# Kernel tuning notes

Hardware: AMD Instinct MI355X
Metric: run time of the kernel (lower is better)

## Reference

```python
import jax, jax.numpy as jnp
import numpy as np

B, S, D, F, E, TOP_K = 4, 2048, 1024, 4096, 8, 2


def setup_inputs() -> dict:
    key = jax.random.key(0)
    ks = jax.random.split(key, 6)
    sd = 1.0 / np.sqrt(D)
    sf = 1.0 / np.sqrt(F)
    return {
        "x": jax.random.normal(ks[0], (B, S, D), dtype=jnp.float32),
        "router_w": jax.random.normal(ks[1], (E, D), dtype=jnp.float32) * sd,
        "router_b": jnp.zeros((E,), dtype=jnp.float32),
        "w1": jax.random.normal(ks[2], (E, F, D), dtype=jnp.float32) * sd,  # Linear(d_model->d_ff) weight [out,in]
        "w2": jax.random.normal(ks[3], (E, D, F), dtype=jnp.float32) * sf,  # Linear(d_ff->d_model)
        "w3": jax.random.normal(ks[4], (E, F, D), dtype=jnp.float32) * sd,
    }


def reference(x, router_w, router_b, w1, w2, w3):
    # Router: softmax over experts, then top-k with renormalized gates.
    logits = jnp.einsum("bsd,ed->bse", x, router_w) + router_b          # [B,S,E]
    probs = jax.nn.softmax(logits, axis=-1)
    topk_p, topk_i = jax.lax.top_k(probs, TOP_K)                         # [B,S,K]
    topk_p = topk_p / jnp.sum(topk_p, axis=-1, keepdims=True)
    # Per-token combine weight for each expert (0 if not selected).
    combine = jnp.sum(jax.nn.one_hot(topk_i, E, dtype=x.dtype) * topk_p[..., None], axis=-2)  # [B,S,E]

    # Note: expert(x*mask)*mask == expert(x)*mask since SwiGLU(0)=0 (no bias).
    out = jnp.zeros_like(x)
    for e in range(E):  # small fixed expert count
        h = jax.nn.silu(jnp.einsum("bsd,fd->bsf", x, w1[e])) * jnp.einsum("bsd,fd->bsf", x, w3[e])
        out = out + combine[..., e:e + 1] * jnp.einsum("bsf,df->bsd", h, w2[e])
    return out
```

## Files before the change

### kernel.cpp

```cpp
#include <hip/hip_runtime.h>
#include <hip/hip_fp16.h>


#define NTOK 8192
#define D_ 1024
#define F_ 4096
#define E_ 8
#define SLOT_CAP 18432

using half8 = __attribute__((ext_vector_type(8))) _Float16;
using half4 = __attribute__((ext_vector_type(4))) _Float16;
using f32x4 = __attribute__((ext_vector_type(4))) float;

__device__ __forceinline__ void gload16(const void* g, void* l) {
  __builtin_amdgcn_global_load_lds((const __attribute__((address_space(1))) void*)g,
                                   (__attribute__((address_space(3))) void*)l, 16, 0, 0);
}

__global__ __launch_bounds__(256) void cvt_kernel(const float* __restrict__ src,
                                                  _Float16* __restrict__ dst, int n4) {
  int i = blockIdx.x * 256 + threadIdx.x;
  int stride = gridDim.x * 256;
  for (; i < n4; i += stride) {
    float4 v = ((const float4*)src)[i];
    half4 h;
    h.x = (_Float16)v.x; h.y = (_Float16)v.y; h.z = (_Float16)v.z; h.w = (_Float16)v.w;
    ((half4*)dst)[i] = h;
  }
}

__global__ __launch_bounds__(256) void cvt_w13_kernel(const float* __restrict__ w1,
                                                      const float* __restrict__ w3,
                                                      _Float16* __restrict__ w13, int n4) {
  int i = blockIdx.x * 256 + threadIdx.x;
  int stride = gridDim.x * 256;
  for (; i < n4; i += stride) {
    int d4 = i & 255;
    int row = i >> 8;
    int e = row >> 12, f = row & 4095;
    size_t vbase = ((size_t)e << 13) | ((size_t)(f >> 4) << 5) | (size_t)(f & 15);
    float4 v1 = ((const float4*)w1)[i];
    float4 v3 = ((const float4*)w3)[i];
    half4 h1, h3;
    h1.x = (_Float16)v1.x; h1.y = (_Float16)v1.y; h1.z = (_Float16)v1.z; h1.w = (_Float16)v1.w;
    h3.x = (_Float16)v3.x; h3.y = (_Float16)v3.y; h3.z = (_Float16)v3.z; h3.w = (_Float16)v3.w;
    ((half4*)w13)[vbase * 256 + d4] = h1;
    ((half4*)w13)[(vbase + 16) * 256 + d4] = h3;
  }
}

__global__ __launch_bounds__(256) void router_kernel(
    const float* __restrict__ x, const float* __restrict__ rw, const float* __restrict__ rbias,
    _Float16* __restrict__ x16, int* __restrict__ tok_e, float* __restrict__ tok_g,
    int* __restrict__ counts) {
  int wv = threadIdx.x >> 6, lane = threadIdx.x & 63;
  int t = blockIdx.x * 4 + wv;
  const float4* xr = (const float4*)(x + (size_t)t * D_);
  float acc[E_];
#pragma unroll
  for (int e = 0; e < E_; ++e) acc[e] = 0.f;
  for (int i = lane; i < D_ / 4; i += 64) {
    float4 xv = xr[i];
    half4 hx;
    hx.x = (_Float16)xv.x; hx.y = (_Float16)xv.y; hx.z = (_Float16)xv.z; hx.w = (_Float16)xv.w;
    ((half4*)(x16 + (size_t)t * D_))[i] = hx;
#pragma unroll
    for (int e = 0; e < E_; ++e) {
      float4 wv4 = ((const float4*)(rw + (size_t)e * D_))[i];
      acc[e] += xv.x * wv4.x + xv.y * wv4.y + xv.z * wv4.z + xv.w * wv4.w;
    }
  }
#pragma unroll
  for (int e = 0; e < E_; ++e) {
#pragma unroll
    for (int off = 32; off > 0; off >>= 1) acc[e] += __shfl_down(acc[e], off);
  }
  if (lane == 0) {
    float p[E_], mx = -1e30f;
#pragma unroll
    for (int e = 0; e < E_; ++e) { p[e] = acc[e] + rbias[e]; mx = fmaxf(mx, p[e]); }
#pragma unroll
    for (int e = 0; e < E_; ++e) p[e] = expf(p[e] - mx);
    int i0 = 0;
#pragma unroll
    for (int e = 1; e < E_; ++e) if (p[e] > p[i0]) i0 = e;
    int i1 = (i0 == 0) ? 1 : 0;
#pragma unroll
    for (int e = 0; e < E_; ++e) if (e != i0 && p[e] > p[i1]) i1 = e;
    float s = p[i0] + p[i1];
    tok_e[t * 2] = i0; tok_e[t * 2 + 1] = i1;
    tok_g[t * 2] = p[i0] / s; tok_g[t * 2 + 1] = p[i1] / s;
    atomicAdd(&counts[i0], 1); atomicAdd(&counts[i1], 1);
  }
}

__global__ void init_kernel(int* slot_token, int* counts, int* cursor) {
  int i = blockIdx.x * 256 + threadIdx.x;
  if (blockIdx.x == 0 && threadIdx.x < E_) { counts[threadIdx.x] = 0; cursor[threadIdx.x] = 0; }
  if (i < SLOT_CAP) slot_token[i] = 0;
}

__global__ void scan_kernel(const int* __restrict__ counts, int* __restrict__ offs) {
  if (threadIdx.x == 0) {
    int o = 0;
    for (int e = 0; e < E_; ++e) { offs[e] = o; o += ((counts[e] + 255) / 256) * 256; }
    offs[E_] = o;
  }
}

__global__ void scatter_kernel(const int* __restrict__ tok_e, const int* __restrict__ offs,
                               int* __restrict__ cursor, int* __restrict__ slot_token,
                               int* __restrict__ slot_of) {
  int i = blockIdx.x * 256 + threadIdx.x;
  if (i >= NTOK * 2) return;
  int e = tok_e[i];
  int pos = offs[e] + atomicAdd(&cursor[e], 1);
  slot_token[pos] = i >> 1;
  slot_of[i] = pos;
}

template <int MODE, int ORD, int KSPLIT, int KD, int NBN, int RPX, int BEROWS>
__global__ __launch_bounds__(512, 2) void moe_gemm_kernel(
    const _Float16* __restrict__ Amat, const _Float16* __restrict__ Bmat,
    const int* __restrict__ slot_token, const int* __restrict__ offs,
    void* __restrict__ outp, void* __restrict__ outp2) {
  constexpr int BM = 256;
  constexpr int MROW = 8;
  constexpr int AH = BM * 32;
  constexpr int BUFH = (BM + 256) * 32;
  constexpr int KL = KD / KSPLIT;
  constexpr int NT = KL / 32;
  __shared__ _Float16 lds[4 * BUFH];

  int id = blockIdx.x;
  int xcd = id & 7, idx = id >> 3;
  int vr, nb;
  if constexpr (ORD == 0) {
    int band = idx / (8 * NBN);
    int i2 = idx - band * (8 * NBN);
    int rib = (RPX - band * 8) < 8 ? (RPX - band * 8) : 8;
    nb = i2 / rib;
    vr = xcd * RPX + band * 8 + (i2 - nb * rib);
  } else {
    nb = idx % NBN;
    vr = xcd * RPX + idx / NBN;
  }
  int rb = vr, ks = 0;
  if constexpr (KSPLIT == 2) { rb = vr >> 1; ks = vr & 1; }
  int row0 = rb * BM;
  if (row0 >= offs[E_]) return;
  int e = 0;
#pragma unroll
  for (int i = 1; i < E_; ++i) if (row0 >= offs[i]) e = i;
  int koff = ks * KL;

  int t = threadIdx.x, l = t & 63, w = t >> 6;
  int wr = w >> 2, wc = w & 3;
  int srow = t >> 2;
  int gsrc8 = ((l & 3) ^ ((l >> 3) & 3)) * 8;

  const _Float16* aP0;
  const _Float16* aP1;
  if constexpr (MODE == 0) {
    int tk0 = slot_token[row0 + srow];
    int tk1 = slot_token[row0 + srow + 128];
    aP0 = Amat + (size_t)tk0 * KD + koff + gsrc8;
    aP1 = Amat + (size_t)tk1 * KD + koff + gsrc8;
  } else {
    aP0 = Amat + (size_t)(row0 + srow) * KD + koff + gsrc8;
    aP1 = Amat + (size_t)(row0 + srow + 128) * KD + koff + gsrc8;
  }
  const _Float16* b0P =
      Bmat + ((size_t)e * BEROWS + (size_t)nb * 256 + srow) * KD + koff + gsrc8;
  const _Float16* b1P = b0P + (size_t)128 * KD;

  int fr = l & 15, kg = l >> 4;
  int swz8 = (kg ^ ((fr >> 1) & 3)) * 8;
  const int rA = (wr * 128 + fr) * 32 + swz8;
  const int rB = AH + (wc * 64 + fr) * 32 + swz8;

  half8 aF[MROW];
  half8 bF[4], bF2[4];
  f32x4 acc[MROW][4];
#pragma unroll
  for (int m = 0; m < MROW; ++m)
#pragma unroll
    for (int n = 0; n < 4; ++n) acc[m][n] = (f32x4){0.f, 0.f, 0.f, 0.f};

#pragma unroll
  for (int tt = 0; tt < 3; ++tt) {
    gload16(aP0 + tt * 32, &lds[tt * BUFH + w * 512]);
    gload16(aP1 + tt * 32, &lds[tt * BUFH + 4096 + w * 512]);
    gload16(b0P + tt * 32, &lds[tt * BUFH + AH + w * 512]);
    gload16(b1P + tt * 32, &lds[tt * BUFH + AH + 4096 + w * 512]);
  }
  asm volatile("s_waitcnt vmcnt(4)" ::: "memory");
  __builtin_amdgcn_s_barrier();
  __builtin_amdgcn_sched_barrier(0);
#pragma unroll
  for (int m = 0; m < MROW; ++m) aF[m] = *(const half8*)&lds[rA + m * 512];
#pragma unroll
  for (int n = 0; n < 4; ++n) bF[n] = *(const half8*)&lds[rB + n * 512];
  __builtin_amdgcn_sched_barrier(0);
  aP0 += 96; aP1 += 96; b0P += 96; b1P += 96;

#define SGB_(m, n) __builtin_amdgcn_sched_group_barrier(m, n, 0)
#define MF4B(mm, BU)                                                                       \
  acc[mm][0] = __builtin_amdgcn_mfma_f32_16x16x32_f16(aF[mm], BU[0], acc[mm][0], 0, 0, 0); \
  acc[mm][1] = __builtin_amdgcn_mfma_f32_16x16x32_f16(aF[mm], BU[1], acc[mm][1], 0, 0, 0); \
  acc[mm][2] = __builtin_amdgcn_mfma_f32_16x16x32_f16(aF[mm], BU[2], acc[mm][2], 0, 0, 0); \
  acc[mm][3] = __builtin_amdgcn_mfma_f32_16x16x32_f16(aF[mm], BU[3], acc[mm][3], 0, 0, 0);

#define GSTEP(U, PRE, WN, BU, BR)                                                 \
  {                                                                               \
    constexpr int bn_ = ((U) + 1) & 3;                                            \
    constexpr int bs_ = ((U) + 3) & 3;                                            \
    __builtin_amdgcn_s_setprio(1);                                                \
    if (PRE) {                                                                    \
      gload16(aP0 + (U) * 32, &lds[bs_ * BUFH + w * 512]);                        \
      gload16(aP1 + (U) * 32, &lds[bs_ * BUFH + 4096 + w * 512]);                 \
      gload16(b0P + (U) * 32, &lds[bs_ * BUFH + AH + w * 512]);                   \
      gload16(b1P + (U) * 32, &lds[bs_ * BUFH + AH + 4096 + w * 512]);            \
    }                                                                             \
    const _Float16* nb_ = &lds[bn_ * BUFH];                                       \
    BR[0] = *(const half8*)(nb_ + rB);                                            \
    BR[1] = *(const half8*)(nb_ + rB + 512);                                      \
    BR[2] = *(const half8*)(nb_ + rB + 1024);                                     \
    BR[3] = *(const half8*)(nb_ + rB + 1536);                                     \
    MF4B(0, BU) aF[0] = *(const half8*)(nb_ + rA);                                \
    MF4B(1, BU) aF[1] = *(const half8*)(nb_ + rA + 512);                          \
    MF4B(2, BU) aF[2] = *(const half8*)(nb_ + rA + 1024);                         \
    MF4B(3, BU) aF[3] = *(const half8*)(nb_ + rA + 1536);                         \
    MF4B(4, BU) aF[4] = *(const half8*)(nb_ + rA + 2048);                         \
    MF4B(5, BU) aF[5] = *(const half8*)(nb_ + rA + 2560);                         \
    MF4B(6, BU) aF[6] = *(const half8*)(nb_ + rA + 3072);                         \
    MF4B(7, BU) aF[7] = *(const half8*)(nb_ + rA + 3584);                         \
    if (PRE) SGB_(0x20, 4);                                                       \
    SGB_(0x100, 4);                                                               \
    SGB_(0x8, 4); SGB_(0x100, 1);                                                 \
    SGB_(0x8, 4); SGB_(0x100, 1);                                                 \
    SGB_(0x8, 4); SGB_(0x100, 1);                                                 \
    SGB_(0x8, 4); SGB_(0x100, 1);                                                 \
    SGB_(0x8, 4); SGB_(0x100, 1);                                                 \
    SGB_(0x8, 4); SGB_(0x100, 1);                                                 \
    SGB_(0x8, 4); SGB_(0x100, 1);                                                 \
    SGB_(0x8, 4); SGB_(0x100, 1);                                                 \
    __builtin_amdgcn_s_setprio(0);                                                \
    if ((WN) >= 0) {                                                              \
      asm volatile("s_waitcnt vmcnt(%0)" ::"i"((WN) >= 0 ? (WN) : 0) : "memory"); \
      __builtin_amdgcn_s_barrier();                                               \
      __builtin_amdgcn_sched_barrier(0);                                          \
    }                                                                             \
  }

  for (int j4 = 0; j4 < NT - 4; j4 += 4) {
    GSTEP(0, true, 4, bF, bF2)
    GSTEP(1, true, 4, bF2, bF)
    GSTEP(2, true, 4, bF, bF2)
    GSTEP(3, true, 4, bF2, bF)
    aP0 += 128; aP1 += 128; b0P += 128; b1P += 128;
  }
  GSTEP(0, true, 4, bF, bF2)
  GSTEP(1, false, 0, bF2, bF)
  GSTEP(2, false, -1, bF, bF2)
  __builtin_amdgcn_s_setprio(1);
  MF4B(0, bF2) MF4B(1, bF2) MF4B(2, bF2) MF4B(3, bF2)
  MF4B(4, bF2) MF4B(5, bF2) MF4B(6, bF2) MF4B(7, bF2)
  __builtin_amdgcn_s_setprio(0);
#undef GSTEP
#undef MF4B
#undef SGB_

  int q4 = kg * 4;
  if constexpr (MODE == 0) {
    _Float16* hb = (_Float16*)outp;
#pragma unroll
    for (int mi = 0; mi < MROW; ++mi) {
      size_t rbase = (size_t)(row0 + wr * 128 + mi * 16 + q4);
#pragma unroll
      for (int p = 0; p < 2; ++p) {
        int fc = nb * 128 + (wc * 2 + p) * 16 + fr;
#pragma unroll
        for (int i = 0; i < 4; ++i) {
          float gv = acc[mi][2 * p][i];
          float hv = gv / (1.f + __expf(-gv)) * acc[mi][2 * p + 1][i];
          hb[(rbase + i) * (size_t)F_ + fc] = (_Float16)hv;
        }
      }
    }
  } else {
    float* yb = (float*)(ks == 0 ? outp : outp2);
#pragma unroll
    for (int mi = 0; mi < MROW; ++mi) {
      size_t rbase = (size_t)(row0 + wr * 128 + mi * 16 + q4);
#pragma unroll
      for (int ni = 0; ni < 4; ++ni) {
        int col = nb * 256 + wc * 64 + ni * 16 + fr;
#pragma unroll
        for (int i = 0; i < 4; ++i)
          yb[(rbase + i) * (size_t)D_ + col] = acc[mi][ni][i];
      }
    }
  }
}

__global__ __launch_bounds__(256) void combine_kernel(
    const float* __restrict__ ya, const float* __restrict__ yb2,
    const int* __restrict__ slot_of, const float* __restrict__ tok_g,
    float* __restrict__ out) {
  int t = blockIdx.x, i = threadIdx.x;
  int s0 = slot_of[t * 2], s1 = slot_of[t * 2 + 1];
  float g0 = tok_g[t * 2], g1 = tok_g[t * 2 + 1];
  float4 a0 = ((const float4*)(ya + (size_t)s0 * D_))[i];
  float4 a1 = ((const float4*)(yb2 + (size_t)s0 * D_))[i];
  float4 b0 = ((const float4*)(ya + (size_t)s1 * D_))[i];
  float4 b1 = ((const float4*)(yb2 + (size_t)s1 * D_))[i];
  float4 r;
  r.x = g0 * (a0.x + a1.x) + g1 * (b0.x + b1.x);
  r.y = g0 * (a0.y + a1.y) + g1 * (b0.y + b1.y);
  r.z = g0 * (a0.z + a1.z) + g1 * (b0.z + b1.z);
  r.w = g0 * (a0.w + a1.w) + g1 * (b0.w + b1.w);
  ((float4*)(out + (size_t)t * D_))[i] = r;
}

extern "C" void kernel_launch(void* const* d_in, const int* in_sizes, int n_in,
                              void* d_out, int out_size, void* d_ws, size_t ws_size,
                              hipStream_t stream) {
  const float* x  = (const float*)d_in[0];
  const float* rw = (const float*)d_in[1];
  const float* rbc = (const float*)d_in[2];
  const float* w1 = (const float*)d_in[3];
  const float* w2 = (const float*)d_in[4];
  const float* w3 = (const float*)d_in[5];
  float* out = (float*)d_out;

  char* ws = (char*)d_ws;
  size_t off = 0;
  auto take = [&](size_t bytes) {
    char* p = ws + off;
    off = (off + bytes + 255) & ~(size_t)255;
    return p;
  };
  _Float16* x16 = (_Float16*)take((size_t)NTOK * D_ * 2);
  _Float16* w13 = (_Float16*)take((size_t)E_ * 2 * F_ * D_ * 2);
  _Float16* w2h = (_Float16*)take((size_t)E_ * D_ * F_ * 2);
  _Float16* hbuf = (_Float16*)take((size_t)SLOT_CAP * F_ * 2);
  float* ybuf = (float*)take((size_t)SLOT_CAP * D_ * 4);
  int* slot_token = (int*)take((size_t)SLOT_CAP * 4);
  int* tok_e = (int*)take((size_t)NTOK * 2 * 4);
  float* tok_g = (float*)take((size_t)NTOK * 2 * 4);
  int* slot_of = (int*)take((size_t)NTOK * 2 * 4);
  int* counts = (int*)take(E_ * 4);
  int* cursor = (int*)take(E_ * 4);
  int* offs = (int*)take((E_ + 1) * 4);
  float* ybuf2 = (float*)w13;

  cvt_w13_kernel<<<4096, 256, 0, stream>>>(w1, w3, w13, E_ * F_ * D_ / 4);
  cvt_kernel<<<4096, 256, 0, stream>>>(w2, w2h, E_ * D_ * F_ / 4);
  init_kernel<<<(SLOT_CAP + 255) / 256, 256, 0, stream>>>(slot_token, counts, cursor);
  router_kernel<<<NTOK / 4, 256, 0, stream>>>(x, rw, rbc, x16, tok_e, tok_g, counts);
  scan_kernel<<<1, 64, 0, stream>>>(counts, offs);
  scatter_kernel<<<(NTOK * 2 + 255) / 256, 256, 0, stream>>>(tok_e, offs, cursor, slot_token, slot_of);
  moe_gemm_kernel<0, 0, 1, 1024, 32, 9, 8192><<<2304, 512, 0, stream>>>(
      x16, w13, slot_token, offs, (void*)hbuf, nullptr);
  moe_gemm_kernel<1, 1, 2, 4096, 4, 18, 1024><<<576, 512, 0, stream>>>(
      hbuf, w2h, slot_token, offs, (void*)ybuf, (void*)ybuf2);
  combine_kernel<<<NTOK, 256, 0, stream>>>(ybuf, ybuf2, slot_of, tok_g, out);
}
```

Baseline: 900.7 us.

## Restructure GEMM main loop into two-phase ping-pong with barriers and reduced fragment registers

Replaces the software-pipelined main loop, which prefetched next-stage A/B fragments interleaved with MFMAs under sched_group_barrier hints, with a two-phase scheme. Each phase loads four A and four B fragments from the current LDS buffer, synchronizes with block barriers and lgkmcnt(0), then issues 16 MFMAs. Global loads are split across the two phases and the vmcnt waits are adjusted to match. This cuts fragment registers (aF 8->4, no double-buffered bF), which may help occupancy, but it adds extra barriers and exposes LDS latency before each MFMA burst.

```diff
diff --git a/kernel.cpp b/kernel.cpp
--- a/kernel.cpp
+++ b/kernel.cpp
@@ -179,8 +179,8 @@
   const int rA = (wr * 128 + fr) * 32 + swz8;
   const int rB = AH + (wc * 64 + fr) * 32 + swz8;
 
-  half8 aF[MROW];
-  half8 bF[4], bF2[4];
+  half8 aF[4];
+  half8 bF[4];
   f32x4 acc[MROW][4];
 #pragma unroll
   for (int m = 0; m < MROW; ++m)
@@ -194,82 +194,79 @@
     gload16(b0P + tt * 32, &lds[tt * BUFH + AH + w * 512]);
     gload16(b1P + tt * 32, &lds[tt * BUFH + AH + 4096 + w * 512]);
   }
-  asm volatile("s_waitcnt vmcnt(4)" ::: "memory");
+  asm volatile("s_waitcnt vmcnt(8)" ::: "memory");
   __builtin_amdgcn_s_barrier();
   __builtin_amdgcn_sched_barrier(0);
-#pragma unroll
-  for (int m = 0; m < MROW; ++m) aF[m] = *(const half8*)&lds[rA + m * 512];
-#pragma unroll
-  for (int n = 0; n < 4; ++n) bF[n] = *(const half8*)&lds[rB + n * 512];
-  __builtin_amdgcn_sched_barrier(0);
   aP0 += 96; aP1 += 96; b0P += 96; b1P += 96;
 
-#define SGB_(m, n) __builtin_amdgcn_sched_group_barrier(m, n, 0)
-#define MF4B(mm, BU)                                                                       \
-  acc[mm][0] = __builtin_amdgcn_mfma_f32_16x16x32_f16(aF[mm], BU[0], acc[mm][0], 0, 0, 0); \
-  acc[mm][1] = __builtin_amdgcn_mfma_f32_16x16x32_f16(aF[mm], BU[1], acc[mm][1], 0, 0, 0); \
-  acc[mm][2] = __builtin_amdgcn_mfma_f32_16x16x32_f16(aF[mm], BU[2], acc[mm][2], 0, 0, 0); \
-  acc[mm][3] = __builtin_amdgcn_mfma_f32_16x16x32_f16(aF[mm], BU[3], acc[mm][3], 0, 0, 0);
-
-#define GSTEP(U, PRE, WN, BU, BR)                                                 \
+#define MF16(BASE)                                                           \
+  _Pragma("unroll") for (int mi = 0; mi < 4; ++mi)                           \
+  _Pragma("unroll") for (int ni = 0; ni < 4; ++ni)                           \
+      acc[(BASE) + mi][ni] = __builtin_amdgcn_mfma_f32_16x16x32_f16(         \
+          aF[mi], bF[ni], acc[(BASE) + mi][ni], 0, 0, 0);
+
+#define STEPP(U, PRE, WN)                                                         \
   {                                                                               \
-    constexpr int bn_ = ((U) + 1) & 3;                                            \
+    constexpr int bi_ = (U) & 3;                                                  \
     constexpr int bs_ = ((U) + 3) & 3;                                            \
-    __builtin_amdgcn_s_setprio(1);                                                \
+    const _Float16* cb_ = &lds[bi_ * BUFH];                                       \
     if (PRE) {                                                                    \
       gload16(aP0 + (U) * 32, &lds[bs_ * BUFH + w * 512]);                        \
       gload16(aP1 + (U) * 32, &lds[bs_ * BUFH + 4096 + w * 512]);                 \
+    }                                                                             \
+    aF[0] = *(const half8*)(cb_ + rA);                                            \
+    aF[1] = *(const half8*)(cb_ + rA + 512);                                      \
+    aF[2] = *(const half8*)(cb_ + rA + 1024);                                     \
+    aF[3] = *(const half8*)(cb_ + rA + 1536);                                     \
+    bF[0] = *(const half8*)(cb_ + rB);                                            \
+    bF[1] = *(const half8*)(cb_ + rB + 512);                                      \
+    bF[2] = *(const half8*)(cb_ + rB + 1024);                                     \
+    bF[3] = *(const half8*)(cb_ + rB + 1536);                                     \
+    __builtin_amdgcn_sched_barrier(0);                                            \
+    __builtin_amdgcn_s_barrier();                                                 \
+    asm volatile("s_waitcnt lgkmcnt(0)" ::: "memory");                            \
+    __builtin_amdgcn_sched_barrier(0);                                            \
+    __builtin_amdgcn_s_setprio(1);                                                \
+    MF16(0)                                                                       \
+    __builtin_amdgcn_s_setprio(0);                                                \
+    __builtin_amdgcn_sched_barrier(0);                                            \
+    __builtin_amdgcn_s_barrier();                                                 \
+    if (PRE) {                                                                    \
       gload16(b0P + (U) * 32, &lds[bs_ * BUFH + AH + w * 512]);                   \
       gload16(b1P + (U) * 32, &lds[bs_ * BUFH + AH + 4096 + w * 512]);            \
     }                                                                             \
-    const _Float16* nb_ = &lds[bn_ * BUFH];                                       \
-    BR[0] = *(const half8*)(nb_ + rB);                                            \
-    BR[1] = *(const half8*)(nb_ + rB + 512);                                      \
-    BR[2] = *(const half8*)(nb_ + rB + 1024);                                     \
-    BR[3] = *(const half8*)(nb_ + rB + 1536);                                     \
-    MF4B(0, BU) aF[0] = *(const half8*)(nb_ + rA);                                \
-    MF4B(1, BU) aF[1] = *(const half8*)(nb_ + rA + 512);                          \
-    MF4B(2, BU) aF[2] = *(const half8*)(nb_ + rA + 1024);                         \
-    MF4B(3, BU) aF[3] = *(const half8*)(nb_ + rA + 1536);                         \
-    MF4B(4, BU) aF[4] = *(const half8*)(nb_ + rA + 2048);                         \
-    MF4B(5, BU) aF[5] = *(const half8*)(nb_ + rA + 2560);                         \
-    MF4B(6, BU) aF[6] = *(const half8*)(nb_ + rA + 3072);                         \
-    MF4B(7, BU) aF[7] = *(const half8*)(nb_ + rA + 3584);                         \
-    if (PRE) SGB_(0x20, 4);                                                       \
-    SGB_(0x100, 4);                                                               \
-    SGB_(0x8, 4); SGB_(0x100, 1);                                                 \
-    SGB_(0x8, 4); SGB_(0x100, 1);                                                 \
-    SGB_(0x8, 4); SGB_(0x100, 1);                                                 \
-    SGB_(0x8, 4); SGB_(0x100, 1);                                                 \
-    SGB_(0x8, 4); SGB_(0x100, 1);                                                 \
-    SGB_(0x8, 4); SGB_(0x100, 1);                                                 \
-    SGB_(0x8, 4); SGB_(0x100, 1);                                                 \
-    SGB_(0x8, 4); SGB_(0x100, 1);                                                 \
+    aF[0] = *(const half8*)(cb_ + rA + 2048);                                     \
+    aF[1] = *(const half8*)(cb_ + rA + 2560);                                     \
+    aF[2] = *(const half8*)(cb_ + rA + 3072);                                     \
+    aF[3] = *(const half8*)(cb_ + rA + 3584);                                     \
+    __builtin_amdgcn_sched_barrier(0);                                            \
+    __builtin_amdgcn_s_barrier();                                                 \
+    asm volatile("s_waitcnt lgkmcnt(0)" ::: "memory");                            \
+    __builtin_amdgcn_sched_barrier(0);                                            \
+    __builtin_amdgcn_s_setprio(1);                                                \
+    MF16(4)                                                                       \
     __builtin_amdgcn_s_setprio(0);                                                \
     if ((WN) >= 0) {                                                              \
       asm volatile("s_waitcnt vmcnt(%0)" ::"i"((WN) >= 0 ? (WN) : 0) : "memory"); \
+      __builtin_amdgcn_sched_barrier(0);                                          \
       __builtin_amdgcn_s_barrier();                                               \
       __builtin_amdgcn_sched_barrier(0);                                          \
     }                                                                             \
   }
 
   for (int j4 = 0; j4 < NT - 4; j4 += 4) {
-    GSTEP(0, true, 4, bF, bF2)
-    GSTEP(1, true, 4, bF2, bF)
-    GSTEP(2, true, 4, bF, bF2)
-    GSTEP(3, true, 4, bF2, bF)
+    STEPP(0, true, 8)
+    STEPP(1, true, 8)
+    STEPP(2, true, 8)
+    STEPP(3, true, 8)
     aP0 += 128; aP1 += 128; b0P += 128; b1P += 128;
   }
-  GSTEP(0, true, 4, bF, bF2)
-  GSTEP(1, false, 0, bF2, bF)
-  GSTEP(2, false, -1, bF, bF2)
-  __builtin_amdgcn_s_setprio(1);
-  MF4B(0, bF2) MF4B(1, bF2) MF4B(2, bF2) MF4B(3, bF2)
-  MF4B(4, bF2) MF4B(5, bF2) MF4B(6, bF2) MF4B(7, bF2)
-  __builtin_amdgcn_s_setprio(0);
-#undef GSTEP
-#undef MF4B
-#undef SGB_
+  STEPP(0, true, 8)
+  STEPP(1, false, 4)
+  STEPP(2, false, 0)
+  STEPP(3, false, -1)
+#undef STEPP
+#undef MF16
 
   int q4 = kg * 4;
   if constexpr (MODE == 0) {
```

Result: no change. 895.2 us (-0.6%).
